# Kernel tuning notes

Measured on AMD Instinct MI355X. Metric: run time of the kernel, lower is better.

The kernel has to match this reference:

```python
import jax, jax.numpy as jnp
import numpy as np

K = 5          # top_k periods
KERNEL = 25    # moving-average kernel for series decomposition
D = 64         # d_model / channels
EPS = 1e-5     # BatchNorm eps (torch default)


def setup_inputs() -> dict:
    key = jax.random.key(0)
    k0, k1, k2, k3, k4 = jax.random.split(key, 5)
    B, T = 8, 2048
    x = jax.random.normal(k0, (B, T, D), jnp.float32)
    w1 = jax.random.normal(k1, (D, D, 3, 3), jnp.float32) * 0.05
    w2 = jax.random.normal(k2, (D, D, 3, 3), jnp.float32) * 0.05
    bn1_gamma = jnp.ones((D,), jnp.float32) + 0.1 * jax.random.normal(k3, (D,), jnp.float32)
    bn2_gamma = jnp.ones((D,), jnp.float32) + 0.1 * jax.random.normal(k4, (D,), jnp.float32)
    z = jnp.zeros((D,), jnp.float32)
    o = jnp.ones((D,), jnp.float32)
    return dict(x=x, w1=w1, w2=w2,
                bn1_gamma=bn1_gamma, bn1_beta=z, bn1_mean=z, bn1_var=o,
                bn2_gamma=bn2_gamma, bn2_beta=z, bn2_mean=z, bn2_var=o)


def _moving_avg(x, kernel):
    # AvgPool1d(stride=1, padding=(kernel-1)//2, count_include_pad=False) over time.
    T = x.shape[1]
    pad = (kernel - 1) // 2
    cs = jnp.concatenate([jnp.zeros_like(x[:, :1]), jnp.cumsum(x, axis=1)], axis=1)  # [B,T+1,C]
    t = jnp.arange(T)
    lo = jnp.clip(t - pad, 0, T)          # inclusive window start
    hi = jnp.clip(t + pad + 1, 0, T)      # exclusive window end
    sums = cs[:, hi] - cs[:, lo]
    return sums / (hi - lo).astype(x.dtype)[None, :, None]


def _auto_corr(s, k):
    T = s.shape[1]
    Xf = jnp.fft.rfft(s, axis=1)
    Pm = (Xf * jnp.conj(Xf)).real.mean(axis=-1)          # [B, T//2+1]
    r = jnp.fft.irfft(Pm, n=T, axis=1)                   # [B, T]
    r = r.at[:, 0].set(-jnp.inf)                          # forbid lag 0
    vals, idx = jax.lax.top_k(r, k)                       # [B,k]
    w = jax.nn.softmax(vals, axis=1)
    return idx, w


def _bn(z, gamma, beta, mean, var):
    return (z - mean) * (gamma * jax.lax.rsqrt(var + EPS)) + beta


def _process_one(s_b, p, w1, w2, bn1, bn2):
    # s_b: [T, C]; p: scalar int period.
    # Equivalent to: roll(s_b, -p), reflect-pad time to cyc*p, fold to [C,cyc,p],
    # Conv2dResBlock (3x3 zero-pad convs + eval BN + GELU + residual), unfold, crop to T.
    T, C = s_b.shape
    U = 2 * T - 2                               # static bound: cyc*p <= T+p-1 <= 2T-2
    u = jnp.arange(U)
    cyc = (T + p - 1) // p
    v = jnp.where(u < T, u, 2 * T - 2 - u)      # reflect extension index
    g = s_b[(v + p) % T]                         # [U,C] rolled-by-(-p) then reflect-padded
    r = u // p                                   # grid row (cycle)
    c = u % p                                    # grid col (phase)

    def conv3x3(z, w):
        # zero-padded 3x3 conv on the [cyc, p] grid, expressed on the flat time axis
        out = jnp.zeros_like(z)
        for dr in (-1, 0, 1):
            for dc in (-1, 0, 1):
                valid = (r + dr >= 0) & (r + dr < cyc) & (c + dc >= 0) & (c + dc < p)
                un = jnp.clip(u + dr * p + dc, 0, U - 1)
                zn = jnp.where(valid[:, None], z[un], 0.0)    # [U,C]
                out = out + zn @ w[:, :, dr + 1, dc + 1].T    # [U,Cout]
        return out

    h = _bn(conv3x3(g, w1), *bn1)
    h = jax.nn.gelu(h, approximate=False)
    h = _bn(conv3x3(h, w2), *bn2)
    return (g + h)[:T]                           # residual + unfold-crop


def reference(x, w1, w2, bn1_gamma, bn1_beta, bn1_mean, bn1_var,
              bn2_gamma, bn2_beta, bn2_mean, bn2_var):
    trend = _moving_avg(x, KERNEL)
    s = x - trend                                # seasonal
    idx, w = _auto_corr(s, K)                    # [B,K] periods, weights
    bn1 = (bn1_gamma, bn1_beta, bn1_mean, bn1_var)
    bn2 = (bn2_gamma, bn2_beta, bn2_mean, bn2_var)
    f = lambda sb, p: _process_one(sb, p, w1, w2, bn1, bn2)
    y = jax.vmap(lambda sb, pb: jax.vmap(lambda p: f(sb, p))(pb))(s, idx)  # [B,K,T,C]
    agg = jnp.einsum('bk,bktc->btc', w, y)
    return agg + trend + x
```

## Files before the change

### kernel.cpp

```cpp
#include <hip/hip_runtime.h>
#include <hip/hip_bf16.h>
#include <math.h>

#define TB 8
#define TT 2048
#define TD 64
#define TK 5
#define TPAD 12
#define EPSBN 1e-5f
#define UMAX 4096

#define ROWS1 128
#define BAND1 130
#define LROWS1 390

#define ROWS2 16
#define BAND2 18
#define LROWS2 54
#define SH8   432
#define BUFB  6912

#define ACG 17

typedef __attribute__((ext_vector_type(8))) short short8;
typedef __attribute__((ext_vector_type(4))) float f32x4;

#define OFF_S     0
#define OFF_SBF   1048576
#define OFF_R     1572864
#define OFF_IDX   1581056
#define OFF_W     1581096
#define OFF_WT1   1581136
#define OFF_WT2   1599568
#define OFF_H1    1618000
#define OFF_CAND  6860880
#define OFF_VALS  6860944

__global__ __launch_bounds__(256) void k_trend(const float* __restrict__ x,
                                               float* __restrict__ out, float* __restrict__ s,
                                               __hip_bfloat16* __restrict__ sbf,
                                               const float* __restrict__ w1, const float* __restrict__ w2,
                                               __hip_bfloat16* __restrict__ wt1, __hip_bfloat16* __restrict__ wt2,
                                               float* __restrict__ r, float* __restrict__ vals)
{
    if (blockIdx.x >= 64) {
        int d = (blockIdx.x - 64) * 256 + threadIdx.x;
        if (d < TB * 1024) r[d] = 0.f;
        if (d < TB * 8) vals[d] = 0.f;
        if (d < 36864) {
            int j = d & 7, l = (d >> 3) & 63, nt = (d >> 9) & 3, kb = d >> 11;
            int tap = kb >> 1, half = kb & 1;
            int co = nt * 16 + (l & 15);
            int ci = half * 32 + (l >> 4) * 8 + j;
            int src = (co * 64 + ci) * 9 + tap;
            wt1[d] = __float2bfloat16(w1[src]);
            wt2[d] = __float2bfloat16(w2[src]);
        }
        return;
    }
    int gid = blockIdx.x * 256 + threadIdx.x;
    int cq = (gid & 15) * 4;
    int tblk = (gid >> 4) & 127;
    int b = gid >> 11;
    int t0 = tblk * 16;
    const float* base = x + (size_t)b * TT * TD + cq;
    float4 sum = make_float4(0.f, 0.f, 0.f, 0.f);
    for (int tt = t0 - TPAD; tt <= t0 + TPAD; ++tt) {
        if (tt >= 0 && tt < TT) {
            float4 v = *(const float4*)(base + (size_t)tt * TD);
            sum.x += v.x; sum.y += v.y; sum.z += v.z; sum.w += v.w;
        }
    }
    size_t o = (size_t)b * TT * TD + (size_t)t0 * TD + cq;
    #pragma unroll
    for (int i = 0; i < 16; ++i) {
        int t = t0 + i;
        int lo = t - TPAD; if (lo < 0) lo = 0;
        int hi = t + TPAD; if (hi > TT - 1) hi = TT - 1;
        float inv = 1.0f / (float)(hi - lo + 1);
        float4 xv = *(const float4*)(base + (size_t)t * TD);
        float4 tr = make_float4(sum.x * inv, sum.y * inv, sum.z * inv, sum.w * inv);
        float4 ov = make_float4(xv.x + tr.x, xv.y + tr.y, xv.z + tr.z, xv.w + tr.w);
        float4 sv = make_float4(xv.x - tr.x, xv.y - tr.y, xv.z - tr.z, xv.w - tr.w);
        *(float4*)(out + o) = ov;
        *(float4*)(s + o) = sv;
        ushort4 us;
        __hip_bfloat16 tb;
        tb = __float2bfloat16(sv.x); us.x = *(unsigned short*)&tb;
        tb = __float2bfloat16(sv.y); us.y = *(unsigned short*)&tb;
        tb = __float2bfloat16(sv.z); us.z = *(unsigned short*)&tb;
        tb = __float2bfloat16(sv.w); us.w = *(unsigned short*)&tb;
        *(ushort4*)((unsigned short*)sbf + o) = us;
        int addt = t + TPAD + 1, subt = t - TPAD;
        if (addt < TT) {
            float4 v = *(const float4*)(base + (size_t)addt * TD);
            sum.x += v.x; sum.y += v.y; sum.z += v.z; sum.w += v.w;
        }
        if (subt >= 0) {
            float4 v = *(const float4*)(base + (size_t)subt * TD);
            sum.x -= v.x; sum.y -= v.y; sum.z -= v.z; sum.w -= v.w;
        }
        o += TD;
    }
}

__global__ __launch_bounds__(256) void k_ac_mfma(const short* __restrict__ sbf16, float* __restrict__ r)
{
    int id = blockIdx.x;
    int b = id & 7;
    int slot = id >> 3;
    int g = slot % ACG;
    int qq = slot / ACG;
    int d0 = g * 4;
    int t0 = qq * 32;
    const short* sb = sbf16 + (size_t)b * TT * TD;

    __shared__ short Atile[2][1024];
    __shared__ short Btile[6][1024];
    __shared__ float scr[4][16 * 17];

    int tid = threadIdx.x;
    if (tid < 128) {
        int dst = (tid * 16) ^ (((tid >> 3) & 7) << 4);
        *(short8*)((char*)Atile[t0 & 1] + dst) =
            *(const short8*)(sb + (size_t)((t0 & 127) * 1024) + tid * 8);
        #pragma unroll
        for (int j = 0; j < 4; ++j) {
            int xi = t0 + d0 + j;
            *(short8*)((char*)Btile[xi % 6] + dst) =
                *(const short8*)(sb + (size_t)((xi & 127) * 1024) + tid * 8);
        }
    }
    __syncthreads();

    int lane = tid & 63, wv = tid >> 6;
    int fr = lane & 15, kg = lane >> 4;
    int roff0 = (fr * 128 + kg * 16) ^ ((fr & 7) << 4);
    int roff1 = roff0 ^ 64;
    int myD = d0 + wv;

    f32x4 acc = {};
    for (int stp = 0; stp < 32; ++stp) {
        int ti = t0 + stp;
        short8 sA, sB;
        if (tid < 128) {
            sA = *(const short8*)(sb + (size_t)(((ti + 1) & 127) * 1024) + tid * 8);
            sB = *(const short8*)(sb + (size_t)(((ti + d0 + 4) & 127) * 1024) + tid * 8);
        }
        const char* Ab = (const char*)Atile[ti & 1];
        const char* Bb = (const char*)Btile[(ti + myD) % 6];
        short8 a0 = *(const short8*)(Ab + roff0);
        short8 a1 = *(const short8*)(Ab + roff1);
        short8 b0 = *(const short8*)(Bb + roff0);
        short8 b1 = *(const short8*)(Bb + roff1);
        acc = __builtin_amdgcn_mfma_f32_16x16x32_bf16(a0, b0, acc, 0, 0, 0);
        acc = __builtin_amdgcn_mfma_f32_16x16x32_bf16(a1, b1, acc, 0, 0, 0);
        if (tid < 128) {
            int dst = (tid * 16) ^ (((tid >> 3) & 7) << 4);
            *(short8*)((char*)Atile[(ti + 1) & 1] + dst) = sA;
            *(short8*)((char*)Btile[(ti + d0 + 4) % 6] + dst) = sB;
        }
        __syncthreads();
    }

    float* sc = scr[wv];
    #pragma unroll
    for (int q = 0; q < 4; ++q)
        sc[(kg * 4 + q) * 17 + fr] = acc[q];
    __syncthreads();
    if (lane < 31) {
        int d = lane - 15;
        int lag = 16 * myD + d;
        if (lag >= 1 && lag <= 1024) {
            int m0 = d < 0 ? -d : 0;
            int m1 = d < 0 ? 16 : 16 - d;
            float v = 0.f;
            for (int m = m0; m < m1; ++m) v += sc[m * 17 + m + d];
            atomicAdd(&r[(size_t)b * 1024 + (lag - 1)], v * (1.0f / 64.0f));
        }
    }
}

__global__ __launch_bounds__(256) void k_cand(const float* __restrict__ r, int* __restrict__ cand)
{
    int b = blockIdx.x;
    __shared__ float v[1024];
    __shared__ float redv[256]; __shared__ int redi[256];
    for (int i = threadIdx.x; i < 1024; i += 256) v[i] = r[(size_t)b * 1024 + i];
    __syncthreads();
    for (int round = 0; round < 8; ++round) {
        float bv = -INFINITY; int bi = 1 << 30;
        for (int i = threadIdx.x; i < 1024; i += 256) {
            float val = v[i];
            if (val > bv) { bv = val; bi = i; }
        }
        redv[threadIdx.x] = bv; redi[threadIdx.x] = bi;
        __syncthreads();
        for (int off = 128; off; off >>= 1) {
            if (threadIdx.x < off) {
                float ov = redv[threadIdx.x + off]; int oi = redi[threadIdx.x + off];
                float mv = redv[threadIdx.x];       int mi = redi[threadIdx.x];
                if (ov > mv || (ov == mv && oi < mi)) { redv[threadIdx.x] = ov; redi[threadIdx.x] = oi; }
            }
            __syncthreads();
        }
        if (threadIdx.x == 0) {
            int lag = redi[0] + 1;
            cand[b * 8 + round] = lag;
            v[lag - 1] = -INFINITY;
        }
        __syncthreads();
    }
}

__global__ __launch_bounds__(256) void k_rescore(const float* __restrict__ s, const int* __restrict__ cand,
                                                 float* __restrict__ vals)
{
    int ci = blockIdx.x;
    int tq = blockIdx.y;
    int b = blockIdx.z;
    int lag = cand[b * 8 + ci];
    const float* sb = s + (size_t)b * TT * TD;
    int cg = (threadIdx.x & 15) * 4;
    int t0 = tq * 512 + (threadIdx.x >> 4) * 32;
    float acc = 0.f;
    #pragma unroll 8
    for (int t = t0; t < t0 + 32; ++t) {
        const float4 a = *(const float4*)(sb + ((size_t)t << 6) + cg);
        const float4 w = *(const float4*)(sb + ((size_t)((t + lag) & (TT - 1)) << 6) + cg);
        acc = fmaf(a.x, w.x, acc);
        acc = fmaf(a.y, w.y, acc);
        acc = fmaf(a.z, w.z, acc);
        acc = fmaf(a.w, w.w, acc);
    }
    __shared__ float red[256];
    red[threadIdx.x] = acc;
    __syncthreads();
    for (int off = 128; off; off >>= 1) {
        if (threadIdx.x < off) red[threadIdx.x] += red[threadIdx.x + off];
        __syncthreads();
    }
    if (threadIdx.x == 0) atomicAdd(&vals[b * 8 + ci], red[0] * (1.0f / 64.0f));
}

__global__ __launch_bounds__(64) void k_sel(const float* __restrict__ vals, const int* __restrict__ cand,
                                            int* __restrict__ selidx, float* __restrict__ selw)
{
    int b = blockIdx.x;
    if (threadIdx.x != 0) return;
    float vv[8]; int ll[8]; bool used[8];
    #pragma unroll
    for (int i = 0; i < 8; ++i) { vv[i] = vals[b * 8 + i]; ll[i] = cand[b * 8 + i]; used[i] = false; }
    int s_idx[6]; float s_val[6]; int slots = 0;
    while (slots < 5) {
        float bv = -INFINITY; int bi = -1;
        for (int i = 0; i < 8; ++i) {
            if (!used[i] && (vv[i] > bv || (vv[i] == bv && bi >= 0 && ll[i] < ll[bi]))) { bv = vv[i]; bi = i; }
        }
        used[bi] = true;
        s_idx[slots] = ll[bi]; s_val[slots] = bv; slots++;
        if (slots < 5 && ll[bi] < 1024) { s_idx[slots] = 2048 - ll[bi]; s_val[slots] = bv; slots++; }
    }
    float mx = -INFINITY;
    for (int i = 0; i < 5; ++i) mx = fmaxf(mx, s_val[i]);
    float e[5], sum = 0.f;
    for (int i = 0; i < 5; ++i) { e[i] = expf(s_val[i] - mx); sum += e[i]; }
    for (int i = 0; i < 5; ++i) { selidx[b * TK + i] = s_idx[i]; selw[b * TK + i] = e[i] / sum; }
}

__global__ __launch_bounds__(256) void k_mm1(
    const short* __restrict__ s_bf, const short* __restrict__ wtp,
    const float* __restrict__ g1, const float* __restrict__ b1,
    const float* __restrict__ m1, const float* __restrict__ v1,
    const int* __restrict__ sel, __hip_bfloat16* __restrict__ h1)
{
    int b = blockIdx.z, k = blockIdx.y;
    int p = sel[b * TK + k];
    int cyc = (TT + p - 1) / p;
    int U = cyc * p;
    int u0 = blockIdx.x * ROWS1;
    if (u0 >= U) return;
    __shared__ short As[LROWS1 * 64];

    const short* sb = s_bf + (size_t)b * TT * TD;
    for (int q = threadIdx.x; q < LROWS1 * 8; q += 256) {
        int row = q >> 3, ch = (q & 7) * 8;
        int band = row / BAND1, i = row - band * BAND1;
        int w = u0 + (band - 1) * p - 1 + i;
        int wc = min(max(w, 0), 2 * TT - 2);
        int v = (wc < TT) ? wc : (2 * TT - 2 - wc);
        int sr = (v + p) & (TT - 1);
        short8 d = *(const short8*)(sb + (size_t)sr * TD + ch);
        int off = (row * 128 + ch * 2) ^ ((row & 7) << 4);
        *(short8*)((char*)As + off) = d;
    }
    __syncthreads();

    int lane = threadIdx.x & 63;
    int wv = threadIdx.x >> 6;
    int lr = lane & 15;
    int kg = lane >> 4;
    int lu[2]; bool inU[2], topf[2], botf[2], leftf[2], rightf[2];
    #pragma unroll
    for (int rs = 0; rs < 2; ++rs) {
        lu[rs] = wv * 32 + rs * 16 + lr;
        int u = u0 + lu[rs];
        inU[rs] = (u < U);
        int r = u / p, c = u - r * p;
        topf[rs] = (r == 0); botf[rs] = (r == cyc - 1);
        leftf[rs] = (c == 0); rightf[rs] = (c == p - 1);
    }

    f32x4 acc[2][4] = {};
    short8 zero = {};
    #pragma unroll
    for (int kb = 0; kb < 18; ++kb) {
        const int tap = kb >> 1, half = kb & 1;
        const int dr = tap / 3 - 1, dc = tap % 3 - 1;
        short8 a[2];
        #pragma unroll
        for (int rs = 0; rs < 2; ++rs) {
            int ldsrow = (dr + 1) * BAND1 + lu[rs] + 1 + dc;
            int off = (ldsrow * 128 + half * 64 + kg * 16) ^ ((ldsrow & 7) << 4);
            a[rs] = *(const short8*)((const char*)As + off);
            bool valid = inU[rs]
                       && !(dr == -1 && topf[rs]) && !(dr == 1 && botf[rs])
                       && !(dc == -1 && leftf[rs]) && !(dc == 1 && rightf[rs]);
            if (!valid) a[rs] = zero;
        }
        #pragma unroll
        for (int nt = 0; nt < 4; ++nt) {
            short8 bq = *(const short8*)(wtp + (size_t)(kb * 4 + nt) * 512 + lane * 8);
            #pragma unroll
            for (int rs = 0; rs < 2; ++rs)
                acc[rs][nt] = __builtin_amdgcn_mfma_f32_16x16x32_bf16(a[rs], bq, acc[rs][nt], 0, 0, 0);
        }
    }
    __hip_bfloat16* ho = h1 + (size_t)(b * TK + k) * (UMAX * TD);
    #pragma unroll
    for (int nt = 0; nt < 4; ++nt) {
        int co = nt * 16 + lr;
        float scale = g1[co] * rsqrtf(v1[co] + EPSBN);
        float bias = b1[co] - m1[co] * scale;
        #pragma unroll
        for (int rs = 0; rs < 2; ++rs) {
            int ub = u0 + wv * 32 + rs * 16 + kg * 4;
            #pragma unroll
            for (int q = 0; q < 4; ++q) {
                int uo = ub + q;
                if (uo < U) {
                    float z = acc[rs][nt][q] * scale + bias;
                    float ge = 0.5f * z * (1.0f + erff(z * 0.70710678118654752f));
                    ho[(size_t)uo * TD + co] = __float2bfloat16(ge);
                }
            }
        }
    }
}

__global__ __launch_bounds__(256) void k_mm2f(
    const short* __restrict__ h1, const short* __restrict__ wtp,
    const float* __restrict__ s,
    const float* __restrict__ g2, const float* __restrict__ b2,
    const float* __restrict__ m2, const float* __restrict__ v2,
    const int* __restrict__ sel, const float* __restrict__ selw,
    float* __restrict__ out)
{
    int b = blockIdx.y;
    int u0 = blockIdx.x * ROWS2;
    int tid = threadIdx.x;
    __shared__ short As[2 * LROWS2 * 64];

    int lane = tid & 63, wv = tid >> 6, lr = lane & 15, kg = lane >> 4;
    int u = u0 + lr;
    const float* sb = s + (size_t)b * TT * TD;

    f32x4 accT = {};
    float gacc[4] = {0.f, 0.f, 0.f, 0.f};
    short8 sreg[2];
    short8 zero = {};

    {
        int p0 = sel[b * TK];
        const short* hb = h1 + (size_t)(b * TK) * (UMAX * TD);
        #pragma unroll
        for (int it = 0; it < 2; ++it) {
            int q = tid + it * 256;
            if (q < SH8) {
                int row = q >> 3, ch = (q & 7) * 8;
                int band = row / BAND2, i = row - band * BAND2;
                int w = u0 + (band - 1) * p0 - 1 + i;
                int wc = min(max(w, 0), UMAX - 1);
                short8 d = *(const short8*)(hb + (size_t)wc * TD + ch);
                int off = (row * 128 + ch * 2) ^ ((row & 7) << 4);
                *(short8*)((char*)As + off) = d;
            }
        }
    }
    __syncthreads();

    for (int k = 0; k < TK; ++k) {
        int p = sel[b * TK + k];
        float wk = selw[b * TK + k];
        int cyc = (TT + p - 1) / p;
        if (k < TK - 1) {
            int pn = sel[b * TK + k + 1];
            const short* hb = h1 + (size_t)(b * TK + k + 1) * (UMAX * TD);
            #pragma unroll
            for (int it = 0; it < 2; ++it) {
                int q = tid + it * 256;
                if (q < SH8) {
                    int row = q >> 3, ch = (q & 7) * 8;
                    int band = row / BAND2, i = row - band * BAND2;
                    int w = u0 + (band - 1) * pn - 1 + i;
                    int wc = min(max(w, 0), UMAX - 1);
                    sreg[it] = *(const short8*)(hb + (size_t)wc * TD + ch);
                }
            }
        }
        const char* Ab = (const char*)As + (k & 1) * BUFB;
        int r = u / p, c = u - r * p;
        bool topf = (r == 0), botf = (r == cyc - 1), leftf = (c == 0), rightf = (c == p - 1);
        f32x4 accP[2] = {};
        #pragma unroll
        for (int kb = 0; kb < 18; ++kb) {
            const int tap = kb >> 1, half = kb & 1;
            const int dr = tap / 3 - 1, dc = tap % 3 - 1;
            int ldsrow = (dr + 1) * BAND2 + lr + 1 + dc;
            int off = (ldsrow * 128 + half * 64 + kg * 16) ^ ((ldsrow & 7) << 4);
            short8 a = *(const short8*)(Ab + off);
            bool valid = !(dr == -1 && topf) && !(dr == 1 && botf)
                       && !(dc == -1 && leftf) && !(dc == 1 && rightf);
            if (!valid) a = zero;
            short8 bq = *(const short8*)(wtp + (size_t)(kb * 4 + wv) * 512 + lane * 8);
            accP[kb & 1] = __builtin_amdgcn_mfma_f32_16x16x32_bf16(a, bq, accP[kb & 1], 0, 0, 0);
        }
        #pragma unroll
        for (int e = 0; e < 4; ++e) accT[e] += wk * (accP[0][e] + accP[1][e]);
        #pragma unroll
        for (int q = 0; q < 4; ++q) {
            int uo = u0 + kg * 4 + q;
            int sr = (uo + p) & (TT - 1);
            gacc[q] = fmaf(wk, sb[(size_t)sr * TD + wv * 16 + lr], gacc[q]);
        }
        __syncthreads();
        if (k < TK - 1) {
            char* Aw = (char*)As + ((k + 1) & 1) * BUFB;
            #pragma unroll
            for (int it = 0; it < 2; ++it) {
                int q = tid + it * 256;
                if (q < SH8) {
                    int row = q >> 3, ch = (q & 7) * 8;
                    int off = (row * 128 + ch * 2) ^ ((row & 7) << 4);
                    *(short8*)(Aw + off) = sreg[it];
                }
            }
            __syncthreads();
        }
    }

    float* ob = out + (size_t)b * TT * TD;
    int co = wv * 16 + lr;
    float scale = g2[co] * rsqrtf(v2[co] + EPSBN);
    float bias = b2[co] - m2[co] * scale;
    #pragma unroll
    for (int q = 0; q < 4; ++q) {
        int uo = u0 + kg * 4 + q;
        size_t idx = (size_t)uo * TD + co;
        ob[idx] = ob[idx] + gacc[q] + scale * accT[q] + bias;
    }
}

extern "C" void kernel_launch(void* const* d_in, const int* in_sizes, int n_in,
                              void* d_out, int out_size, void* d_ws, size_t ws_size,
                              hipStream_t stream)
{
    const float* x  = (const float*)d_in[0];
    const float* w1 = (const float*)d_in[1];
    const float* w2 = (const float*)d_in[2];
    const float* g1 = (const float*)d_in[3];
    const float* b1 = (const float*)d_in[4];
    const float* m1 = (const float*)d_in[5];
    const float* v1 = (const float*)d_in[6];
    const float* g2 = (const float*)d_in[7];
    const float* b2 = (const float*)d_in[8];
    const float* m2 = (const float*)d_in[9];
    const float* v2 = (const float*)d_in[10];

    float* ws    = (float*)d_ws;
    float* s     = ws + OFF_S;
    __hip_bfloat16* sbf = (__hip_bfloat16*)(ws + OFF_SBF);
    float* r     = ws + OFF_R;
    int*   sel   = (int*)(ws + OFF_IDX);
    float* selw  = ws + OFF_W;
    __hip_bfloat16* wt1 = (__hip_bfloat16*)(ws + OFF_WT1);
    __hip_bfloat16* wt2 = (__hip_bfloat16*)(ws + OFF_WT2);
    __hip_bfloat16* h1  = (__hip_bfloat16*)(ws + OFF_H1);
    int*   cand  = (int*)(ws + OFF_CAND);
    float* vals  = ws + OFF_VALS;
    float* out   = (float*)d_out;

    k_trend   <<<dim3(208),         dim3(256), 0, stream>>>(x, out, s, sbf, w1, w2, wt1, wt2, r, vals);
    k_ac_mfma <<<dim3(544),         dim3(256), 0, stream>>>((const short*)sbf, r);
    k_cand    <<<dim3(TB),          dim3(256), 0, stream>>>(r, cand);
    k_rescore <<<dim3(8, 4, TB),    dim3(256), 0, stream>>>(s, cand, vals);
    k_sel     <<<dim3(TB),          dim3(64),  0, stream>>>(vals, cand, sel, selw);
    k_mm1     <<<dim3(32, TK, TB),  dim3(256), 0, stream>>>((const short*)sbf, (const short*)wt1,
                                                            g1, b1, m1, v1, sel, h1);
    k_mm2f    <<<dim3(128, TB),     dim3(256), 0, stream>>>((const short*)h1, (const short*)wt2, s,
                                                            g2, b2, m2, v2, sel, selw, out);
}
```

Before: 115.5 us.

## Process two time steps per barrier in autocorrelation MFMA kernel with deeper buffers

```diff
diff --git a/kernel.cpp b/kernel.cpp
--- a/kernel.cpp
+++ b/kernel.cpp
@@ -115,19 +115,21 @@
     int t0 = qq * 32;
     const short* sb = sbf16 + (size_t)b * TT * TD;
 
-    __shared__ short Atile[2][1024];
-    __shared__ short Btile[6][1024];
+    __shared__ short Atile[4][1024];
+    __shared__ short Btile[8][1024];
     __shared__ float scr[4][16 * 17];
 
     int tid = threadIdx.x;
     if (tid < 128) {
         int dst = (tid * 16) ^ (((tid >> 3) & 7) << 4);
-        *(short8*)((char*)Atile[t0 & 1] + dst) =
-            *(const short8*)(sb + (size_t)((t0 & 127) * 1024) + tid * 8);
-        #pragma unroll
-        for (int j = 0; j < 4; ++j) {
+        #pragma unroll
+        for (int j = 0; j < 2; ++j)
+            *(short8*)((char*)Atile[(t0 + j) & 3] + dst) =
+                *(const short8*)(sb + (size_t)(((t0 + j) & 127) * 1024) + tid * 8);
+        #pragma unroll
+        for (int j = 0; j < 5; ++j) {
             int xi = t0 + d0 + j;
-            *(short8*)((char*)Btile[xi % 6] + dst) =
+            *(short8*)((char*)Btile[xi & 7] + dst) =
                 *(const short8*)(sb + (size_t)((xi & 127) * 1024) + tid * 8);
         }
     }
@@ -139,27 +141,40 @@
     int roff1 = roff0 ^ 64;
     int myD = d0 + wv;
 
+    int ch0 = (tid & 63) * 2;
+    int dstc0 = (ch0 * 16) ^ (((ch0 >> 3) & 7) << 4);
+    int dstc1 = ((ch0 + 1) * 16) ^ ((((ch0 + 1) >> 3) & 7) << 4);
+
     f32x4 acc = {};
-    for (int stp = 0; stp < 32; ++stp) {
-        int ti = t0 + stp;
-        short8 sA, sB;
-        if (tid < 128) {
-            sA = *(const short8*)(sb + (size_t)(((ti + 1) & 127) * 1024) + tid * 8);
-            sB = *(const short8*)(sb + (size_t)(((ti + d0 + 4) & 127) * 1024) + tid * 8);
-        }
-        const char* Ab = (const char*)Atile[ti & 1];
-        const char* Bb = (const char*)Btile[(ti + myD) % 6];
-        short8 a0 = *(const short8*)(Ab + roff0);
-        short8 a1 = *(const short8*)(Ab + roff1);
-        short8 b0 = *(const short8*)(Bb + roff0);
-        short8 b1 = *(const short8*)(Bb + roff1);
-        acc = __builtin_amdgcn_mfma_f32_16x16x32_bf16(a0, b0, acc, 0, 0, 0);
-        acc = __builtin_amdgcn_mfma_f32_16x16x32_bf16(a1, b1, acc, 0, 0, 0);
-        if (tid < 128) {
-            int dst = (tid * 16) ^ (((tid >> 3) & 7) << 4);
-            *(short8*)((char*)Atile[(ti + 1) & 1] + dst) = sA;
-            *(short8*)((char*)Btile[(ti + d0 + 4) % 6] + dst) = sB;
-        }
+    for (int it = 0; it < 16; ++it) {
+        int ti = t0 + 2 * it;
+        int grow = (wv == 0) ? (ti + 2) : (wv == 1) ? (ti + 3)
+                 : (wv == 2) ? (ti + d0 + 5) : (ti + d0 + 6);
+        const short* srcp = sb + (size_t)((grow & 127) * 1024);
+        short8 sv0 = *(const short8*)(srcp + ch0 * 8);
+        short8 sv1 = *(const short8*)(srcp + ch0 * 8 + 8);
+        {
+            const char* Ab = (const char*)Atile[ti & 3];
+            const char* Bb = (const char*)Btile[(ti + myD) & 7];
+            short8 a0 = *(const short8*)(Ab + roff0);
+            short8 a1 = *(const short8*)(Ab + roff1);
+            short8 b0 = *(const short8*)(Bb + roff0);
+            short8 b1 = *(const short8*)(Bb + roff1);
+            acc = __builtin_amdgcn_mfma_f32_16x16x32_bf16(a0, b0, acc, 0, 0, 0);
+            acc = __builtin_amdgcn_mfma_f32_16x16x32_bf16(a1, b1, acc, 0, 0, 0);
+            const char* Ab2 = (const char*)Atile[(ti + 1) & 3];
+            const char* Bb2 = (const char*)Btile[(ti + 1 + myD) & 7];
+            a0 = *(const short8*)(Ab2 + roff0);
+            a1 = *(const short8*)(Ab2 + roff1);
+            b0 = *(const short8*)(Bb2 + roff0);
+            b1 = *(const short8*)(Bb2 + roff1);
+            acc = __builtin_amdgcn_mfma_f32_16x16x32_bf16(a0, b0, acc, 0, 0, 0);
+            acc = __builtin_amdgcn_mfma_f32_16x16x32_bf16(a1, b1, acc, 0, 0, 0);
+        }
+        char* dsttile = (wv == 0) ? (char*)Atile[(ti + 2) & 3] : (wv == 1) ? (char*)Atile[(ti + 3) & 3]
+                      : (wv == 2) ? (char*)Btile[(ti + d0 + 5) & 7] : (char*)Btile[(ti + d0 + 6) & 7];
+        *(short8*)(dsttile + dstc0) = sv0;
+        *(short8*)(dsttile + dstc1) = sv1;
         __syncthreads();
     }
 
```

New measurement: 116.7 us. No clear change (+1.1%).
